# Kernel optimization log

Measured on AMD Instinct MI355X. Metric: run time of the kernel, lower is better.

The kernel has to match this reference:

```python
import jax, jax.numpy as jnp
import numpy as np

D_MODEL = 1024
BASE = 7
NUM_PLANES = 2
EPS = 1e-6


def setup_inputs() -> dict:
    key = jax.random.key(0)
    k_x, k_w, k_t, k_g = jax.random.split(key, 4)
    B, S, D = 4, 8192, D_MODEL
    x = jax.random.normal(k_x, (B, S, D), dtype=jnp.float32)
    # eidosTransform params: linear 3D -> D, then 2 planes of learned rotation angles over D/2 pairs
    W = jax.random.normal(k_w, (3 * D, D), dtype=jnp.float32) / np.sqrt(3 * D)
    b = jnp.zeros((D,), dtype=jnp.float32)
    theta = jax.random.normal(k_t, (NUM_PLANES, D // 2), dtype=jnp.float32) * 0.1
    # ModularPhaseNorm gain
    gamma = jnp.ones((D,), dtype=jnp.float32)
    return {"x": x, "W": W, "b": b, "theta": theta, "gamma": gamma}


def _eidos_transform(t, W, b, theta):
    # linear projection 3D -> D ('truncate' collapse to d_out)
    y = jnp.einsum("bse,ed->bsd", t, W) + b  # [B,S,D]
    B, S, D = y.shape
    # geometric mode: rotate (even, odd) dim pairs by learned angles, per plane
    for p in range(NUM_PLANES):
        yp = y.reshape(B, S, D // 2, 2)
        a, c2 = yp[..., 0], yp[..., 1]
        cos_t = jnp.cos(theta[p])
        sin_t = jnp.sin(theta[p])
        ra = a * cos_t - c2 * sin_t
        rb = a * sin_t + c2 * cos_t
        y = jnp.stack([ra, rb], axis=-1).reshape(B, S, D)
    return y


def _modular_phase_norm(y, gamma):
    # RMS-normalize within feature groups defined by (dim index mod BASE)
    D = y.shape[-1]
    group = jnp.arange(D) % BASE                      # [D]
    onehot = jax.nn.one_hot(group, BASE, dtype=y.dtype)  # [D, BASE]
    counts = onehot.sum(axis=0)                       # [BASE]
    ss = jnp.einsum("bsd,dg->bsg", y * y, onehot)     # [B,S,BASE]
    rms = jnp.sqrt(ss / counts + EPS)                 # [B,S,BASE]
    denom = rms[..., group]                           # [B,S,D]
    return y / denom * gamma


def reference(x, W, b, theta, gamma):
    B, S, D = x.shape
    zero_row = jnp.zeros((B, 1, D), dtype=x.dtype)
    left = jnp.concatenate([zero_row, x[:, :-1, :]], axis=1)   # roll +1, zero first
    right = jnp.concatenate([x[:, 1:, :], zero_row], axis=1)   # roll -1, zero last
    triplet = jnp.concatenate([left, x, right], axis=-1)        # [B,S,3D]
    mixed = _eidos_transform(triplet, W, b, theta)
    return _modular_phase_norm(mixed, gamma)
```

## Files before the change

kernel.cpp:

```cpp
#include <hip/hip_runtime.h>
#include <hip/hip_bf16.h>
#include <stdint.h>


#define SEQ 8192
#define NB 4
#define DM 1024
#define KD 3072

typedef __attribute__((ext_vector_type(8))) short short8_t;
typedef __attribute__((ext_vector_type(4))) float f32x4;

__device__ __forceinline__ unsigned short f2bf(float f) {
  union { float f; uint32_t u; } v; v.f = f;
  return (unsigned short)((v.u + 0x7fffu + ((v.u >> 16) & 1u)) >> 16);
}

__device__ __forceinline__ void async_ld16(const void* g, void* l) {
  __builtin_amdgcn_global_load_lds(
      (const __attribute__((address_space(1))) uint32_t*)g,
      (__attribute__((address_space(3))) uint32_t*)(uint32_t)(uintptr_t)l,
      16, 0, 0);
}

__global__ __launch_bounds__(256) void prep_w(const float* __restrict__ W,
                                              const float* __restrict__ theta,
                                              unsigned short* __restrict__ Wt) {
  __shared__ float csc[32], css[32];
  __shared__ unsigned short tile[64][72];
  const int bk = blockIdx.x % 48, bn = blockIdx.x / 48;
  const int k0 = bk * 64, n0 = bn * 64;
  const int t = threadIdx.x;
  if (t < 32) {
    int d = n0 / 2 + t;
    float ang = theta[d] + theta[512 + d];
    csc[t] = cosf(ang); css[t] = sinf(ang);
  }
  __syncthreads();
#pragma unroll
  for (int i = 0; i < 8; ++i) {
    int idx = i * 256 + t;
    int pr = idx >> 5;
    int pc = idx & 31;
    const float2 w2 = *(const float2*)&W[(size_t)(k0 + pr) * DM + n0 + pc * 2];
    float c = csc[pc], s = css[pc];
    tile[pc * 2][pr]     = f2bf(w2.x * c - w2.y * s);
    tile[pc * 2 + 1][pr] = f2bf(w2.x * s + w2.y * c);
  }
  __syncthreads();
#pragma unroll
  for (int i = 0; i < 16; ++i) {
    int idx = i * 256 + t;
    int r = idx >> 6, cdx = idx & 63;
    Wt[(size_t)(n0 + r) * KD + k0 + cdx] = tile[r][cdx];
  }
}

__global__ void prep_bias(const float* __restrict__ b, const float* __restrict__ theta,
                          float* __restrict__ biasp, float* __restrict__ zp) {
  const int t = threadIdx.x;
  float ang = theta[t] + theta[512 + t];
  float c = cosf(ang), s = sinf(ang);
  float be = b[2 * t], bo = b[2 * t + 1];
  biasp[2 * t]     = be * c - bo * s;
  biasp[2 * t + 1] = be * s + bo * c;
  if (t < 256) ((float4*)zp)[t] = make_float4(0.f, 0.f, 0.f, 0.f);
}

__global__ __launch_bounds__(256) void prep_x(const float* __restrict__ x,
                                              unsigned short* __restrict__ xbp) {
  const size_t total = (size_t)NB * 8194 * 128;
  for (size_t i = (size_t)blockIdx.x * 256 + threadIdx.x; i < total;
       i += (size_t)gridDim.x * 256) {
    int d8 = (int)(i & 127);
    size_t rem = i >> 7;
    int sp = (int)(rem % 8194);
    size_t bb = rem / 8194;
    uint4 o = make_uint4(0u, 0u, 0u, 0u);
    if (sp > 0 && sp < 8193) {
      const float4* src = (const float4*)(x + (bb * SEQ + (size_t)(sp - 1)) * DM + d8 * 8);
      float4 lo = src[0], hi = src[1];
      o.x = (uint32_t)f2bf(lo.x) | ((uint32_t)f2bf(lo.y) << 16);
      o.y = (uint32_t)f2bf(lo.z) | ((uint32_t)f2bf(lo.w) << 16);
      o.z = (uint32_t)f2bf(hi.x) | ((uint32_t)f2bf(hi.y) << 16);
      o.w = (uint32_t)f2bf(hi.z) | ((uint32_t)f2bf(hi.w) << 16);
    }
    ((uint4*)xbp)[i] = o;
  }
}

__global__ __launch_bounds__(512, 2) void gemm256(const unsigned short* __restrict__ xbp,
                                                  const unsigned short* __restrict__ Wt,
                                                  const float* __restrict__ biasp,
                                                  float* __restrict__ out) {
  __shared__ __align__(16) unsigned char As[4][16384];
  __shared__ __align__(16) unsigned char Bs[4][16384];

  const int tid = threadIdx.x;
  const int lane = tid & 63;
  const int wid = tid >> 6;
  const int wm = wid >> 2, wn = wid & 3;
  const int row16 = lane & 15, kgrp = lane >> 4;

  const int L = blockIdx.x;
  const int xcd = L & 7;
  const int j = L >> 3;
  const int mtile = xcd * 16 + (j >> 2);
  const int ntile = j & 3;

  const int n0 = ntile * 256;
  const int batch = mtile >> 5;
  const int s0 = (mtile & 31) * 256;
  const size_t m0 = (size_t)mtile * 256;

  int aoff[8], boff[4];
#pragma unroll
  for (int mi = 0; mi < 4; ++mi) {
    int r = wm * 128 + mi * 16 + row16;
    aoff[mi] = r * 64 + (kgrp ^ ((r >> 1) & 3)) * 16;
    int r2 = r + 64;
    aoff[mi + 4] = r2 * 64 + (kgrp ^ ((r2 >> 1) & 3)) * 16;
  }
#pragma unroll
  for (int ni = 0; ni < 4; ++ni) {
    int r = wn * 64 + ni * 16 + row16;
    boff[ni] = r * 64 + (kgrp ^ ((r >> 1) & 3)) * 16;
  }

  auto stageA = [&](int kt, int buf) {
    const int c = kt >> 5;
    const int ksb = (kt & 31) * 32;
    const size_t base = ((size_t)batch * 8194 + (size_t)(s0 + c)) * DM + ksb;
#pragma unroll
    for (int i = 0; i < 2; ++i) {
      int idx = i * 512 + tid;
      int row = idx >> 2, c16 = idx & 3;
      int cs = c16 ^ ((row >> 1) & 3);
      async_ld16(xbp + base + (size_t)row * DM + cs * 8, &As[buf][idx * 16]);
    }
  };
  auto stageB = [&](int kt, int buf) {
    const int kb = kt * 32;
#pragma unroll
    for (int i = 0; i < 2; ++i) {
      int idx = i * 512 + tid;
      int row = idx >> 2, c16 = idx & 3;
      int cs = c16 ^ ((row >> 1) & 3);
      async_ld16(Wt + (size_t)(n0 + row) * KD + kb + cs * 8, &Bs[buf][idx * 16]);
    }
  };

  f32x4 acc[8][4];
#pragma unroll
  for (int a = 0; a < 8; ++a)
#pragma unroll
    for (int b = 0; b < 4; ++b) acc[a][b] = (f32x4){0.f, 0.f, 0.f, 0.f};

  short8_t afA[4], bfA[4], afB[4], bfB[4], af1[4];

  stageA(0, 0); stageB(0, 0);
  stageA(1, 1); stageB(1, 1);
  stageA(2, 2); stageB(2, 2);
  asm volatile("s_waitcnt vmcnt(4)" ::: "memory");
  __builtin_amdgcn_s_barrier();
#pragma unroll
  for (int mi = 0; mi < 4; ++mi) afA[mi] = *(const short8_t*)(&As[0][0] + aoff[mi]);
#pragma unroll
  for (int ni = 0; ni < 4; ++ni) bfA[ni] = *(const short8_t*)(&Bs[0][0] + boff[ni]);
  __builtin_amdgcn_sched_barrier(0);

  auto body = [&](int kt, int buf, int doStage, int doNext, int vm4,
                  short8_t (&afC)[4], short8_t (&bfC)[4],
                  short8_t (&afN)[4], short8_t (&bfN)[4]) {
    const int nbuf = (buf + 1) & 3, sbuf = (buf + 3) & 3;
    if (doStage) { stageA(kt + 3, sbuf); stageB(kt + 3, sbuf); }
#pragma unroll
    for (int mi = 0; mi < 4; ++mi)
      af1[mi] = *(const short8_t*)(&As[buf][0] + aoff[mi + 4]);
    asm volatile("s_waitcnt lgkmcnt(4)" ::: "memory");
    __builtin_amdgcn_sched_barrier(0);
    __builtin_amdgcn_s_setprio(1);
#pragma unroll
    for (int mi = 0; mi < 4; ++mi)
#pragma unroll
      for (int ni = 0; ni < 4; ++ni)
        acc[mi][ni] = __builtin_amdgcn_mfma_f32_16x16x32_bf16(
            afC[mi], bfC[ni], acc[mi][ni], 0, 0, 0);
    __builtin_amdgcn_s_setprio(0);
    __builtin_amdgcn_sched_barrier(0);
    if (doNext) {
#pragma unroll
      for (int mi = 0; mi < 4; ++mi)
        afN[mi] = *(const short8_t*)(&As[nbuf][0] + aoff[mi]);
#pragma unroll
      for (int ni = 0; ni < 4; ++ni)
        bfN[ni] = *(const short8_t*)(&Bs[nbuf][0] + boff[ni]);
    }
    if (doNext) asm volatile("s_waitcnt lgkmcnt(8)" ::: "memory");
    else        asm volatile("s_waitcnt lgkmcnt(0)" ::: "memory");
    __builtin_amdgcn_sched_barrier(0);
    __builtin_amdgcn_s_setprio(1);
#pragma unroll
    for (int mi = 0; mi < 4; ++mi)
#pragma unroll
      for (int ni = 0; ni < 4; ++ni)
        acc[mi + 4][ni] = __builtin_amdgcn_mfma_f32_16x16x32_bf16(
            af1[mi], bfC[ni], acc[mi + 4][ni], 0, 0, 0);
    __builtin_amdgcn_s_setprio(0);
    if (vm4) asm volatile("s_waitcnt vmcnt(4)" ::: "memory");
    else     asm volatile("s_waitcnt vmcnt(0)" ::: "memory");
    __builtin_amdgcn_sched_barrier(0);
    __builtin_amdgcn_s_barrier();
  };

  for (int kt4 = 0; kt4 < 92; kt4 += 4) {
    body(kt4 + 0, 0, 1, 1, 1, afA, bfA, afB, bfB);
    body(kt4 + 1, 1, 1, 1, 1, afB, bfB, afA, bfA);
    body(kt4 + 2, 2, 1, 1, 1, afA, bfA, afB, bfB);
    body(kt4 + 3, 3, 1, 1, 1, afB, bfB, afA, bfA);
  }
  body(92, 0, 1, 1, 1, afA, bfA, afB, bfB);
  body(93, 1, 0, 1, 0, afB, bfB, afA, bfA);
  body(94, 2, 0, 1, 0, afA, bfA, afB, bfB);
  body(95, 3, 0, 0, 0, afB, bfB, afA, bfA);
  asm volatile("s_waitcnt lgkmcnt(0)" ::: "memory");

#pragma unroll
  for (int mi = 0; mi < 8; ++mi) {
    size_t grow = m0 + (size_t)(wm * 128 + mi * 16 + kgrp * 4);
#pragma unroll
    for (int ni = 0; ni < 4; ++ni) {
      int col = n0 + wn * 64 + ni * 16 + row16;
      float bia = biasp[col];
      float* op = out + grow * DM + col;
#pragma unroll
      for (int r = 0; r < 4; ++r) op[(size_t)r * DM] = acc[mi][ni][r] + bia;
    }
  }
}

__global__ __launch_bounds__(256) void gemm_fb(const float* __restrict__ Ag,
                                               const unsigned short* __restrict__ Wt,
                                               const float* __restrict__ biasp,
                                               const float* __restrict__ zp,
                                               float* __restrict__ out) {
  __shared__ __align__(16) unsigned char As[128 * 64 * 4];
  __shared__ __align__(16) unsigned char Bs[128 * 64 * 2];

  const int tid = threadIdx.x;
  const int lane = tid & 63;
  const int wid = tid >> 6;
  const int wm = wid >> 1, wn = wid & 1;
  const int row16 = lane & 15, kgrp = lane >> 4;

  const int L = blockIdx.x;
  const int xcd = L & 7;
  const int j = L >> 3;
  const int mtile = xcd * 32 + (j >> 3);
  const int ntile = j & 7;

  const int n0 = ntile * 128;
  const int batch = mtile >> 6;
  const int s0 = (mtile & 63) * 128;
  const size_t m0 = (size_t)mtile * 128;

  f32x4 acc[4][4];
#pragma unroll
  for (int a = 0; a < 4; ++a)
#pragma unroll
    for (int b = 0; b < 4; ++b) acc[a][b] = (f32x4){0.f, 0.f, 0.f, 0.f};

  for (int kt = 0; kt < 48; ++kt) {
    const int c = kt >> 4;
    const int ksb = (kt & 15) * 64;
    __syncthreads();
#pragma unroll
    for (int it = 0; it < 8; ++it) {
      int f16 = it * 256 + tid;
      int row = f16 >> 4, c16 = f16 & 15;
      int c16s = c16 ^ (row & 7);
      int s = s0 + row + c - 1;
      const float* src = (s >= 0 && s < SEQ)
          ? Ag + ((size_t)batch * SEQ + (size_t)s) * DM + ksb + c16s * 4
          : zp + c16s * 4;
      async_ld16(src, As + f16 * 16);
    }
#pragma unroll
    for (int it = 0; it < 4; ++it) {
      int f16 = it * 256 + tid;
      int row = f16 >> 3, c16 = f16 & 7;
      int c16s = c16 ^ (row & 7);
      const unsigned short* src = Wt + (size_t)(n0 + row) * KD + kt * 64 + c16s * 8;
      async_ld16(src, Bs + f16 * 16);
    }
    __syncthreads();

#pragma unroll
    for (int kk = 0; kk < 2; ++kk) {
      short8_t af[4], bfr[4];
#pragma unroll
      for (int mi = 0; mi < 4; ++mi) {
        int r = wm * 64 + mi * 16 + row16;
        int kb = kk * 128 + kgrp * 32;
        f32x4 lo = *(const f32x4*)(As + r * 256 + (kb ^ ((r & 7) << 4)));
        f32x4 hi = *(const f32x4*)(As + r * 256 + ((kb + 16) ^ ((r & 7) << 4)));
        union { short8_t v; unsigned short u[8]; } pk;
        pk.u[0] = f2bf(lo[0]); pk.u[1] = f2bf(lo[1]);
        pk.u[2] = f2bf(lo[2]); pk.u[3] = f2bf(lo[3]);
        pk.u[4] = f2bf(hi[0]); pk.u[5] = f2bf(hi[1]);
        pk.u[6] = f2bf(hi[2]); pk.u[7] = f2bf(hi[3]);
        af[mi] = pk.v;
      }
#pragma unroll
      for (int ni = 0; ni < 4; ++ni) {
        int r = wn * 64 + ni * 16 + row16;
        int kb = kk * 64 + kgrp * 16;
        bfr[ni] = *(const short8_t*)(Bs + r * 128 + (kb ^ ((r & 7) << 4)));
      }
#pragma unroll
      for (int mi = 0; mi < 4; ++mi)
#pragma unroll
        for (int ni = 0; ni < 4; ++ni)
          acc[mi][ni] = __builtin_amdgcn_mfma_f32_16x16x32_bf16(
              af[mi], bfr[ni], acc[mi][ni], 0, 0, 0);
    }
  }

#pragma unroll
  for (int mi = 0; mi < 4; ++mi) {
    size_t grow = m0 + (size_t)(wm * 64 + mi * 16 + kgrp * 4);
#pragma unroll
    for (int ni = 0; ni < 4; ++ni) {
      int col = n0 + wn * 64 + ni * 16 + row16;
      float bia = biasp[col];
      float* op = out + grow * DM + col;
#pragma unroll
      for (int r = 0; r < 4; ++r) op[(size_t)r * DM] = acc[mi][ni][r] + bia;
    }
  }
}

__global__ __launch_bounds__(256) void norm_kernel(float* __restrict__ y,
                                                   const float* __restrict__ gamma) {
  const int tid = threadIdx.x, lane = tid & 63, wv = tid >> 6;
  const size_t row = (size_t)blockIdx.x * 4 + wv;
  float4* rp = (float4*)(y + row * DM);
  const float4* gp = (const float4*)gamma;
  float4 v[4];
#pragma unroll
  for (int jj = 0; jj < 4; ++jj) v[jj] = rp[jj * 64 + lane];

  float ss[7] = {0.f, 0.f, 0.f, 0.f, 0.f, 0.f, 0.f};
#pragma unroll
  for (int jj = 0; jj < 4; ++jj) {
    const float vv[4] = {v[jj].x, v[jj].y, v[jj].z, v[jj].w};
#pragma unroll
    for (int i = 0; i < 4; ++i) {
      int d = (jj * 64 + lane) * 4 + i;
      int g = d % 7;
      float sq = vv[i] * vv[i];
#pragma unroll
      for (int t = 0; t < 7; ++t) ss[t] += (g == t) ? sq : 0.f;
    }
  }
#pragma unroll
  for (int t = 0; t < 7; ++t) {
#pragma unroll
    for (int off = 32; off >= 1; off >>= 1) ss[t] += __shfl_xor(ss[t], off, 64);
  }
  float inv[7];
#pragma unroll
  for (int t = 0; t < 7; ++t) {
    float cnt = (t < 2) ? 147.f : 146.f;
    inv[t] = rsqrtf(ss[t] / cnt + 1e-6f);
  }
#pragma unroll
  for (int jj = 0; jj < 4; ++jj) {
    float4 g4 = gp[jj * 64 + lane];
    const float vv[4] = {v[jj].x, v[jj].y, v[jj].z, v[jj].w};
    const float gg[4] = {g4.x, g4.y, g4.z, g4.w};
    float o[4];
#pragma unroll
    for (int i = 0; i < 4; ++i) {
      int d = (jj * 64 + lane) * 4 + i;
      int g = d % 7;
      float iv = inv[0];
#pragma unroll
      for (int t = 1; t < 7; ++t) iv = (g == t) ? inv[t] : iv;
      o[i] = vv[i] * iv * gg[i];
    }
    rp[jj * 64 + lane] = make_float4(o[0], o[1], o[2], o[3]);
  }
}

extern "C" void kernel_launch(void* const* d_in, const int* in_sizes, int n_in,
                              void* d_out, int out_size, void* d_ws, size_t ws_size,
                              hipStream_t stream) {
  const float* x     = (const float*)d_in[0];
  const float* W     = (const float*)d_in[1];
  const float* b     = (const float*)d_in[2];
  const float* theta = (const float*)d_in[3];
  const float* gamma = (const float*)d_in[4];
  float* out = (float*)d_out;
  (void)in_sizes; (void)n_in; (void)out_size;

  char* ws = (char*)d_ws;
  unsigned short* Wt = (unsigned short*)ws;
  float* biasp = (float*)(ws + 6291456);
  float* zp    = (float*)(ws + 6291456 + 4096);
  unsigned short* xbp = (unsigned short*)(ws + 6299648);
  const size_t needA = 6299648 + (size_t)NB * 8194 * DM * 2;

  prep_w<<<dim3(768), dim3(256), 0, stream>>>(W, theta, Wt);
  prep_bias<<<dim3(1), dim3(512), 0, stream>>>(b, theta, biasp, zp);

  if (ws_size >= needA) {
    prep_x<<<dim3(4096), dim3(256), 0, stream>>>(x, xbp);
    gemm256<<<dim3(512), dim3(512), 0, stream>>>(xbp, Wt, biasp, out);
  } else {
    gemm_fb<<<dim3(2048), dim3(256), 0, stream>>>(x, Wt, biasp, zp, out);
  }
  norm_kernel<<<dim3(8192), dim3(256), 0, stream>>>(out, gamma);
}
```

Measured before the change: 260.3 us.

## Load GEMM A fragments directly from global memory, dropping the A LDS staging

The A operand (bf16 shifted input) is no longer staged through LDS. Each wave now loads its MFMA A fragments straight from global memory into registers, prefetching one k-step ahead, while B keeps the 4-buffer LDS pipeline. The vmcnt/lgkmcnt waits are reworked to match the new mix of outstanding global and LDS loads. This frees 64KB of LDS and removes the LDS write/read for A. The cost is that rows are re-fetched from global/L2 by the waves sharing them, with uncoalesced 16-byte strided accesses, and global latency may become exposed before the MFMAs.

```diff
diff --git a/kernel.cpp b/kernel.cpp
--- a/kernel.cpp
+++ b/kernel.cpp
@@ -93,7 +93,6 @@
                                                   const unsigned short* __restrict__ Wt,
                                                   const float* __restrict__ biasp,
                                                   float* __restrict__ out) {
-  __shared__ __align__(16) unsigned char As[4][16384];
   __shared__ __align__(16) unsigned char Bs[4][16384];
 
   const int tid = threadIdx.x;
@@ -113,32 +112,21 @@
   const int s0 = (mtile & 31) * 256;
   const size_t m0 = (size_t)mtile * 256;
 
-  int aoff[8], boff[4];
+  size_t arow[8];
 #pragma unroll
   for (int mi = 0; mi < 4; ++mi) {
-    int r = wm * 128 + mi * 16 + row16;
-    aoff[mi] = r * 64 + (kgrp ^ ((r >> 1) & 3)) * 16;
-    int r2 = r + 64;
-    aoff[mi + 4] = r2 * 64 + (kgrp ^ ((r2 >> 1) & 3)) * 16;
-  }
+    arow[mi] = (size_t)(wm * 128 + mi * 16 + row16) * DM + kgrp * 8;
+    arow[mi + 4] = arow[mi] + (size_t)64 * DM;
+  }
+  const size_t abase0 = ((size_t)batch * 8194 + (size_t)s0) * DM;
+
+  int boff[4];
 #pragma unroll
   for (int ni = 0; ni < 4; ++ni) {
     int r = wn * 64 + ni * 16 + row16;
     boff[ni] = r * 64 + (kgrp ^ ((r >> 1) & 3)) * 16;
   }
 
-  auto stageA = [&](int kt, int buf) {
-    const int c = kt >> 5;
-    const int ksb = (kt & 31) * 32;
-    const size_t base = ((size_t)batch * 8194 + (size_t)(s0 + c)) * DM + ksb;
-#pragma unroll
-    for (int i = 0; i < 2; ++i) {
-      int idx = i * 512 + tid;
-      int row = idx >> 2, c16 = idx & 3;
-      int cs = c16 ^ ((row >> 1) & 3);
-      async_ld16(xbp + base + (size_t)row * DM + cs * 8, &As[buf][idx * 16]);
-    }
-  };
   auto stageB = [&](int kt, int buf) {
     const int kb = kt * 32;
 #pragma unroll
@@ -156,28 +144,48 @@
 #pragma unroll
     for (int b = 0; b < 4; ++b) acc[a][b] = (f32x4){0.f, 0.f, 0.f, 0.f};
 
-  short8_t afA[4], bfA[4], afB[4], bfB[4], af1[4];
-
-  stageA(0, 0); stageB(0, 0);
-  stageA(1, 1); stageB(1, 1);
-  stageA(2, 2); stageB(2, 2);
+  short8_t af0A[4], af0B[4], bfA[4], bfB[4], af1r[4];
+
+  stageB(0, 0); stageB(1, 1); stageB(2, 2);
+  {
+    const size_t kb0 = abase0;
+#pragma unroll
+    for (int mi = 0; mi < 4; ++mi)
+      af0A[mi] = *(const short8_t*)(xbp + kb0 + arow[mi]);
+  }
   asm volatile("s_waitcnt vmcnt(4)" ::: "memory");
   __builtin_amdgcn_s_barrier();
 #pragma unroll
-  for (int mi = 0; mi < 4; ++mi) afA[mi] = *(const short8_t*)(&As[0][0] + aoff[mi]);
-#pragma unroll
   for (int ni = 0; ni < 4; ++ni) bfA[ni] = *(const short8_t*)(&Bs[0][0] + boff[ni]);
   __builtin_amdgcn_sched_barrier(0);
 
-  auto body = [&](int kt, int buf, int doStage, int doNext, int vm4,
-                  short8_t (&afC)[4], short8_t (&bfC)[4],
-                  short8_t (&afN)[4], short8_t (&bfN)[4]) {
+  auto body = [&](int kt, int buf, int doStage, int doNextA, int doNextB,
+                  int vmTop, int vmMid, int lgTop,
+                  short8_t (&af0C)[4], short8_t (&bfC)[4],
+                  short8_t (&af0N)[4], short8_t (&bfN)[4]) {
     const int nbuf = (buf + 1) & 3, sbuf = (buf + 3) & 3;
-    if (doStage) { stageA(kt + 3, sbuf); stageB(kt + 3, sbuf); }
+    const int c = kt >> 5, ksb = (kt & 31) * 32;
+    const size_t kbase = abase0 + (size_t)c * DM + ksb;
 #pragma unroll
     for (int mi = 0; mi < 4; ++mi)
-      af1[mi] = *(const short8_t*)(&As[buf][0] + aoff[mi + 4]);
-    asm volatile("s_waitcnt lgkmcnt(4)" ::: "memory");
+      af1r[mi] = *(const short8_t*)(xbp + kbase + arow[mi + 4]);
+    __builtin_amdgcn_sched_barrier(0);
+    if (doStage) stageB(kt + 3, sbuf);
+    if (doNextA) {
+      const int c2 = (kt + 1) >> 5, ksb2 = ((kt + 1) & 31) * 32;
+      const size_t kbase2 = abase0 + (size_t)c2 * DM + ksb2;
+#pragma unroll
+      for (int mi = 0; mi < 4; ++mi)
+        af0N[mi] = *(const short8_t*)(xbp + kbase2 + arow[mi]);
+    }
+    if (doNextB) {
+#pragma unroll
+      for (int ni = 0; ni < 4; ++ni)
+        bfN[ni] = *(const short8_t*)(&Bs[nbuf][0] + boff[ni]);
+    }
+    if (vmTop == 8)      asm volatile("s_waitcnt vmcnt(8) lgkmcnt(4)" ::: "memory");
+    else if (lgTop == 4) asm volatile("s_waitcnt vmcnt(4) lgkmcnt(4)" ::: "memory");
+    else                 asm volatile("s_waitcnt vmcnt(4) lgkmcnt(0)" ::: "memory");
     __builtin_amdgcn_sched_barrier(0);
     __builtin_amdgcn_s_setprio(1);
 #pragma unroll
@@ -185,19 +193,11 @@
 #pragma unroll
       for (int ni = 0; ni < 4; ++ni)
         acc[mi][ni] = __builtin_amdgcn_mfma_f32_16x16x32_bf16(
-            afC[mi], bfC[ni], acc[mi][ni], 0, 0, 0);
+            af0C[mi], bfC[ni], acc[mi][ni], 0, 0, 0);
     __builtin_amdgcn_s_setprio(0);
-    __builtin_amdgcn_sched_barrier(0);
-    if (doNext) {
-#pragma unroll
-      for (int mi = 0; mi < 4; ++mi)
-        afN[mi] = *(const short8_t*)(&As[nbuf][0] + aoff[mi]);
-#pragma unroll
-      for (int ni = 0; ni < 4; ++ni)
-        bfN[ni] = *(const short8_t*)(&Bs[nbuf][0] + boff[ni]);
-    }
-    if (doNext) asm volatile("s_waitcnt lgkmcnt(8)" ::: "memory");
-    else        asm volatile("s_waitcnt lgkmcnt(0)" ::: "memory");
+    if (vmMid == 6)      asm volatile("s_waitcnt vmcnt(6)" ::: "memory");
+    else if (vmMid == 4) asm volatile("s_waitcnt vmcnt(4)" ::: "memory");
+    else                 asm volatile("s_waitcnt vmcnt(0)" ::: "memory");
     __builtin_amdgcn_sched_barrier(0);
     __builtin_amdgcn_s_setprio(1);
 #pragma unroll
@@ -205,25 +205,22 @@
 #pragma unroll
       for (int ni = 0; ni < 4; ++ni)
         acc[mi + 4][ni] = __builtin_amdgcn_mfma_f32_16x16x32_bf16(
-            af1[mi], bfC[ni], acc[mi + 4][ni], 0, 0, 0);
+            af1r[mi], bfC[ni], acc[mi + 4][ni], 0, 0, 0);
     __builtin_amdgcn_s_setprio(0);
-    if (vm4) asm volatile("s_waitcnt vmcnt(4)" ::: "memory");
-    else     asm volatile("s_waitcnt vmcnt(0)" ::: "memory");
     __builtin_amdgcn_sched_barrier(0);
     __builtin_amdgcn_s_barrier();
   };
 
   for (int kt4 = 0; kt4 < 92; kt4 += 4) {
-    body(kt4 + 0, 0, 1, 1, 1, afA, bfA, afB, bfB);
-    body(kt4 + 1, 1, 1, 1, 1, afB, bfB, afA, bfA);
-    body(kt4 + 2, 2, 1, 1, 1, afA, bfA, afB, bfB);
-    body(kt4 + 3, 3, 1, 1, 1, afB, bfB, afA, bfA);
-  }
-  body(92, 0, 1, 1, 1, afA, bfA, afB, bfB);
-  body(93, 1, 0, 1, 0, afB, bfB, afA, bfA);
-  body(94, 2, 0, 1, 0, afA, bfA, afB, bfB);
-  body(95, 3, 0, 0, 0, afB, bfB, afA, bfA);
-  asm volatile("s_waitcnt lgkmcnt(0)" ::: "memory");
+    body(kt4 + 0, 0, 1, 1, 1, 8, 6, 4, af0A, bfA, af0B, bfB);
+    body(kt4 + 1, 1, 1, 1, 1, 8, 6, 4, af0B, bfB, af0A, bfA);
+    body(kt4 + 2, 2, 1, 1, 1, 8, 6, 4, af0A, bfA, af0B, bfB);
+    body(kt4 + 3, 3, 1, 1, 1, 8, 6, 4, af0B, bfB, af0A, bfA);
+  }
+  body(92, 0, 1, 1, 1, 8, 6, 4, af0A, bfA, af0B, bfB);
+  body(93, 1, 0, 1, 1, 8, 4, 4, af0B, bfB, af0A, bfA);
+  body(94, 2, 0, 1, 1, 8, 4, 4, af0A, bfA, af0B, bfB);
+  body(95, 3, 0, 0, 0, 4, 0, 0, af0B, bfB, af0A, bfA);
 
 #pragma unroll
   for (int mi = 0; mi < 8; ++mi) {
```

After: 531.6 us. 2.04x slower.
